# Optimization experiments

Measured on AMD Instinct MI355X. Metric: run time of the kernel, lower is better.

## Reference

```python
import jax, jax.numpy as jnp
import numpy as np

THR = 0.5      # span-selection threshold
K_SUBJ = 16    # max subject/object spans kept per sentence (padded)
K_OBJ = 8      # max object spans kept per (subject, relation)

# Greedy threshold-based span pairing: for each start position i with
# start_prob>THR, take the first unused j>=i with end_prob>THR (NMS-like).
# Returns fixed-size padded spans [K,2] (int32) and a validity mask [K].
def greedy_spans(sp, ep, K):
    S = sp.shape[0]
    idxs = jnp.arange(S, dtype=jnp.int32)
    def step(carry, i):
        used, count, spans, valid = carry
        gate = sp[i] > THR
        cand = (ep > THR) & (~used) & (idxs >= i)
        has = jnp.any(cand)
        j = jnp.argmax(cand).astype(jnp.int32)  # first True
        found = gate & has
        slot = jnp.minimum(count, K - 1)
        write = found & (count < K)
        pair = jnp.where(write, jnp.stack([i, j]).astype(jnp.int32), spans[slot])
        spans = spans.at[slot].set(pair)
        valid = valid.at[slot].set(valid[slot] | write)
        used = used.at[j].set(used[j] | found)
        count = count + found.astype(jnp.int32)
        return (used, count, spans, valid), None
    init = (jnp.zeros(S, bool), jnp.int32(0),
            jnp.zeros((K, 2), jnp.int32), jnp.zeros(K, bool))
    (_, _, spans, valid), _ = jax.lax.scan(step, init, idxs)
    return spans, valid


def _model(token_embs, hg, rel_embs, b_rel_transe, head_w, head_b,
           Wmats, Wbias, rproj_w, rproj_b, V_w, V_b):
    # head_w/head_b order: 0 start_subj, 1 end_subj, 2 b_start_obj, 3 b_end_obj,
    #                      4 start_obj, 5 end_obj, 6 b_start_subj, 7 b_end_subj
    # Wmats/Wbias order:   0 W_s, 1 W_r, 2 W_g, 3 W_x, 4 W_r_b, 5 W_g_b, 6 W_x_b, 7 W_x2
    sig = jax.nn.sigmoid
    head = lambda x, i: sig(x @ head_w[i] + head_b[i])        # H->1 sigmoid head
    lin = lambda x, i: x @ Wmats[i].T + Wbias[i]              # H->H linear

    # ---- first-level span scores + greedy extraction (forward & backward) ----
    sub_sp, sub_ep = head(token_embs, 0), head(token_embs, 1)   # [B,S]
    bob_sp, bob_ep = head(token_embs, 2), head(token_embs, 3)
    g = jax.vmap(lambda a, b: greedy_spans(a, b, K_SUBJ))
    subj_spans, subj_valid = g(sub_sp, sub_ep)                  # [B,K,2],[B,K]
    b_subj_spans, b_subj_valid = g(bob_sp, bob_ep)

    def gather(tok_b, spans, valid):  # mean of start/end token embeddings
        e = (tok_b[spans[:, 0]] + tok_b[spans[:, 1]]) * 0.5
        return e * valid[:, None].astype(tok_b.dtype)
    s_k = jax.vmap(gather)(token_embs, subj_spans, subj_valid)      # [B,K,H]
    b_s_k = jax.vmap(gather)(token_embs, b_subj_spans, b_subj_valid)
    s_k_w = lin(s_k, 0) * subj_valid[..., None]                     # W_s + mask
    b_s_k_w = lin(b_s_k, 0) * b_subj_valid[..., None]

    # ---- relation-aware attention context C = sum_s A[b,s,r] * x[b,s] ----
    b_rel = b_rel_transe @ rproj_w.T + rproj_b                      # r_proj
    def attend(rels, ir, ig, ix):
        e = jnp.tanh(lin(token_embs, ix)[:, :, None, :]             # [B,S,1,H]
                     + lin(hg, ig)[:, None, None, :]                # [B,1,1,H]
                     + lin(rels, ir)[None, None, :, :])             # [1,1,R,H]
        v = e @ V_w + V_b[0]                                        # [B,S,R]
        A = jax.nn.softmax(v, axis=1)                               # over seq
        return jnp.einsum('bsr,bsh->brh', A, token_embs)            # [B,R,H]
    C = attend(rel_embs, 1, 2, 3)
    b_C = attend(b_rel, 4, 5, 6)

    # Heads are linear, so distribute w over the sum instead of
    # materializing the [B,S,K,R,H] tensor.
    tok_mix = token_embs + lin(token_embs, 7)
    def pair_probs(Cmat, skw, i):
        t_tok = tok_mix @ head_w[i]                                 # [B,S]
        t_sub = skw @ head_w[i]                                     # [B,K]
        t_rel = Cmat @ head_w[i]                                    # [B,R]
        return sig(t_tok[:, :, None, None] + t_sub[:, None, :, None]
                   + t_rel[:, None, None, :] + head_b[i])           # [B,S,K,R]
    obj_sp, obj_ep = pair_probs(C, s_k_w, 4), pair_probs(C, s_k_w, 5)
    bsub_sp, bsub_ep = pair_probs(b_C, b_s_k_w, 6), pair_probs(b_C, b_s_k_w, 7)

    # ---- greedy object-span extraction per (batch, subject, relation) ----
    def triples(sp4, ep4, subj_ok):
        B_, S_, K_, R_ = sp4.shape
        fsp = sp4.transpose(0, 2, 3, 1).reshape(-1, S_)
        fep = ep4.transpose(0, 2, 3, 1).reshape(-1, S_)
        spans, valid = jax.vmap(lambda a, b: greedy_spans(a, b, K_OBJ))(fsp, fep)
        spans = spans.reshape(B_, K_, R_, K_OBJ, 2)
        valid = valid.reshape(B_, K_, R_, K_OBJ) & subj_ok[:, :, None, None]
        return spans, valid
    f_spans, f_valid = triples(obj_sp, obj_ep, subj_valid)
    bw_spans, bw_valid = triples(bsub_sp, bsub_ep, b_subj_valid)

    probs = jnp.stack([obj_sp, obj_ep, bsub_sp, bsub_ep])           # [4,B,S,K,R]
    return (probs, subj_spans, subj_valid, b_subj_spans, b_subj_valid,
            f_spans, f_valid, bw_spans, bw_valid)


def setup_inputs() -> dict:
    key = jax.random.key(0)
    ks = jax.random.split(key, 12)
    B, S, H, R, T = 8, 256, 768, 40, 80
    sc = H ** -0.5
    return {
        'token_embs': jax.random.normal(ks[0], (B, S, H), jnp.float32),
        'hg': jax.random.normal(ks[1], (B, H), jnp.float32),
        'rel_embs': jax.random.normal(ks[2], (R, H), jnp.float32),
        'b_rel_transe': jax.random.normal(ks[3], (R, T), jnp.float32),
        'head_w': jax.random.normal(ks[4], (8, H), jnp.float32) * sc,
        'head_b': jax.random.normal(ks[5], (8,), jnp.float32) * 0.1,
        'Wmats': jax.random.normal(ks[6], (8, H, H), jnp.float32) * sc,
        'Wbias': jax.random.normal(ks[7], (8, H), jnp.float32) * 0.02,
        'rproj_w': jax.random.normal(ks[8], (H, T), jnp.float32) * (T ** -0.5),
        'rproj_b': jax.random.normal(ks[9], (H,), jnp.float32) * 0.02,
        'V_w': jax.random.normal(ks[10], (H,), jnp.float32) * sc,
        'V_b': jax.random.normal(ks[11], (1,), jnp.float32) * 0.1,
    }


def reference(token_embs, hg, rel_embs, b_rel_transe, head_w, head_b,
              Wmats, Wbias, rproj_w, rproj_b, V_w, V_b):
    return _model(token_embs, hg, rel_embs, b_rel_transe, head_w, head_b,
                  Wmats, Wbias, rproj_w, rproj_b, V_w, V_b)
```

## Files before the change

### kernel.cpp

```cpp
#include <hip/hip_runtime.h>
#include <hip/hip_bf16.h>
#include <stdint.h>

#define Bc 8
#define Sc 256
#define Hc 768
#define Rc 40
#define Tc 80
#define KSc 16
#define KOc 8

#define OUT_SSP 5242880
#define OUT_SVA 5243136
#define OUT_BSP 5243264
#define OUT_BVA 5243520
#define OUT_FSP 5243648
#define OUT_FVA 5325568
#define OUT_WSP 5366528
#define OUT_WVA 5448448

#define CM_PS (16 * Rc * Hc)
#define BSH (Bc * Sc * Hc)

__device__ inline double wave_reduce_d(double v) {
#pragma unroll
  for (int o = 32; o; o >>= 1) v += __shfl_down(v, o, 64);
  return v;
}
__device__ inline float wave_reduce_f(float v) {
#pragma unroll
  for (int o = 32; o; o >>= 1) v += __shfl_down(v, o, 64);
  return v;
}

__global__ __launch_bounds__(256) void k_l03(const float* __restrict__ x,
                                             const float* __restrict__ head_w,
                                             const float* __restrict__ head_b,
                                             float* __restrict__ l03) {
  int bs = blockIdx.x * 4 + (threadIdx.x >> 6);
  int lane = threadIdx.x & 63;
  if (bs >= Bc * Sc) return;
  const float* xr = x + (size_t)bs * Hc;
  double acc[4] = {0.0, 0.0, 0.0, 0.0};
  for (int h = lane; h < Hc; h += 64) {
    double xv = (double)xr[h];
    acc[0] += xv * (double)head_w[h];
    acc[1] += xv * (double)head_w[Hc + h];
    acc[2] += xv * (double)head_w[2 * Hc + h];
    acc[3] += xv * (double)head_w[3 * Hc + h];
  }
#pragma unroll
  for (int i = 0; i < 4; ++i) {
    double a = wave_reduce_d(acc[i]);
    if (lane == 0) l03[i * (Bc * Sc) + bs] = (float)(a + (double)head_b[i]);
  }
}

__device__ inline int find_first(const uint64_t* epm, const uint64_t* used, int i) {
  int wi = i >> 6;
  uint64_t m = epm[wi] & ~used[wi] & (~0ull << (i & 63));
  if (m) return (wi << 6) + (__ffsll((unsigned long long)m) - 1);
  for (int w = wi + 1; w < 4; ++w) {
    uint64_t mm = epm[w] & ~used[w];
    if (mm) return (w << 6) + (__ffsll((unsigned long long)mm) - 1);
  }
  return -1;
}

__global__ __launch_bounds__(64) void k_greedy1(const float* __restrict__ l03,
                                                int* __restrict__ spans1, int* __restrict__ valid1,
                                                float* __restrict__ out) {
  int t = blockIdx.x;
  int dir = t >> 3, b = t & 7;
  int lane = threadIdx.x;
  const float* sp = l03 + (dir * 2) * (Bc * Sc) + b * Sc;
  const float* ep = sp + Bc * Sc;
  uint64_t spm[4], epm[4];
#pragma unroll
  for (int w = 0; w < 4; ++w) {
    spm[w] = __ballot(sp[w * 64 + lane] > 0.f);
    epm[w] = __ballot(ep[w * 64 + lane] > 0.f);
  }
  __shared__ int ssp0[KSc], ssp1[KSc], sva[KSc];
  if (lane < KSc) { ssp0[lane] = 0; ssp1[lane] = 0; sva[lane] = 0; }
  __syncthreads();
  if (lane == 0) {
    uint64_t used[4] = {0, 0, 0, 0};
    int cnt = 0;
#pragma unroll
    for (int w = 0; w < 4; ++w) {
      uint64_t g = spm[w];
      while (g) {
        int bit = __ffsll((unsigned long long)g) - 1;
        g &= g - 1;
        int i = w * 64 + bit;
        int j = find_first(epm, used, i);
        if (j < 0) continue;
        used[j >> 6] |= (1ull << (j & 63));
        if (cnt < KSc) { ssp0[cnt] = i; ssp1[cnt] = j; sva[cnt] = 1; }
        cnt++;
      }
    }
  }
  __syncthreads();
  int base = (dir * Bc + b) * KSc;
  float* osp = out + (dir ? OUT_BSP : OUT_SSP) + b * KSc * 2;
  float* ova = out + (dir ? OUT_BVA : OUT_SVA) + b * KSc;
  if (lane < KSc) {
    spans1[(base + lane) * 2] = ssp0[lane];
    spans1[(base + lane) * 2 + 1] = ssp1[lane];
    valid1[base + lane] = sva[lane];
    osp[lane * 2] = (float)ssp0[lane];
    osp[lane * 2 + 1] = (float)ssp1[lane];
    ova[lane] = (float)sva[lane];
  }
}

__global__ __launch_bounds__(256) void k_prep(const float* __restrict__ brt,
                                              const float* __restrict__ rw,
                                              const float* __restrict__ rb,
                                              const float* __restrict__ Wmats,
                                              const float* __restrict__ head_w,
                                              const float* __restrict__ x,
                                              const int* __restrict__ spans1,
                                              float* __restrict__ brel,
                                              double* __restrict__ hv,
                                              float* __restrict__ eb) {
  int bb = blockIdx.x;
  int tid = threadIdx.x;
  if (bb < 12) {
    int idx = bb * 256 + tid;
    int i = idx / Hc, j = idx % Hc;
    const float* h4 = head_w + (4 + i) * Hc;
    const float* W7 = Wmats + (size_t)7 * Hc * Hc;
    double acc = (double)h4[j];
    for (int hh = 0; hh < Hc; ++hh)
      acc += (double)W7[(size_t)hh * Hc + j] * (double)h4[hh];
    hv[idx] = acc;
  } else if (bb < 132) {
    int idx = (bb - 12) * 256 + tid;
    int r = idx / Hc, h = idx % Hc;
    float acc = rb[h];
    const float* a = brt + r * Tc;
    const float* w = rw + (size_t)h * Tc;
    for (int t = 0; t < Tc; ++t) acc = fmaf(a[t], w[t], acc);
    brel[idx] = acc;
  } else {
    int row = bb - 132;
    int b = (row / KSc) % Bc;
    int s0 = spans1[row * 2], s1 = spans1[row * 2 + 1];
    const float* x0 = x + ((size_t)b * Sc + s0) * Hc;
    const float* x1 = x + ((size_t)b * Sc + s1) * Hc;
    float* er = eb + (size_t)row * Hc;
    for (int h = tid; h < Hc; h += 256) er[h] = 0.5f * (x0[h] + x1[h]);
  }
}

__global__ __launch_bounds__(256) void k_skw(const float* __restrict__ eb,
                                             const float* __restrict__ Wmats,
                                             const float* __restrict__ Wbias,
                                             const int* __restrict__ valid1,
                                             float* __restrict__ skw) {
  int m0 = blockIdx.y * 32;
  int n0 = blockIdx.x * 64;
  __shared__ float Asl[32][36];
  __shared__ float Bsl[32][68];
  int tid = threadIdx.x;
  int arow = tid >> 3, acol = (tid & 7) << 2;
  int brow = tid >> 2, bcol = (tid & 3) << 2;
  int txi = tid & 15, tyi = tid >> 4;
  const float* ap = eb + (size_t)(m0 + arow) * Hc + acol;
  const float* bp = Wmats + (size_t)(n0 + brow) * Hc + bcol;
  int nb = n0 + txi * 4;
  float4 bias = *(const float4*)&Wbias[nb];
  float acc[2][4];
#pragma unroll
  for (int i = 0; i < 2; ++i) { acc[i][0] = bias.x; acc[i][1] = bias.y; acc[i][2] = bias.z; acc[i][3] = bias.w; }
  for (int k0 = 0; k0 < Hc; k0 += 32) {
    float4 av = *(const float4*)(ap + k0);
    float4 b0 = *(const float4*)(bp + k0);
    float4 b1 = *(const float4*)(bp + k0 + 16);
    __syncthreads();
    Asl[acol + 0][arow] = av.x; Asl[acol + 1][arow] = av.y; Asl[acol + 2][arow] = av.z; Asl[acol + 3][arow] = av.w;
    Bsl[bcol + 0][brow] = b0.x; Bsl[bcol + 1][brow] = b0.y; Bsl[bcol + 2][brow] = b0.z; Bsl[bcol + 3][brow] = b0.w;
    Bsl[bcol + 16][brow] = b1.x; Bsl[bcol + 17][brow] = b1.y; Bsl[bcol + 18][brow] = b1.z; Bsl[bcol + 19][brow] = b1.w;
    __syncthreads();
#pragma unroll
    for (int kk = 0; kk < 32; ++kk) {
      float a0 = Asl[kk][tyi * 2], a1 = Asl[kk][tyi * 2 + 1];
      float4 b = *(const float4*)&Bsl[kk][txi * 4];
      acc[0][0] = fmaf(a0, b.x, acc[0][0]); acc[0][1] = fmaf(a0, b.y, acc[0][1]);
      acc[0][2] = fmaf(a0, b.z, acc[0][2]); acc[0][3] = fmaf(a0, b.w, acc[0][3]);
      acc[1][0] = fmaf(a1, b.x, acc[1][0]); acc[1][1] = fmaf(a1, b.y, acc[1][1]);
      acc[1][2] = fmaf(a1, b.z, acc[1][2]); acc[1][3] = fmaf(a1, b.w, acc[1][3]);
    }
  }
  int m_ = m0 + tyi * 2;
#pragma unroll
  for (int i = 0; i < 2; ++i) {
    int v = valid1[m_ + i];
    float4 o;
    o.x = v ? acc[i][0] : 0.f; o.y = v ? acc[i][1] : 0.f;
    o.z = v ? acc[i][2] : 0.f; o.w = v ? acc[i][3] : 0.f;
    *(float4*)&skw[(size_t)(m_ + i) * Hc + nb] = o;
  }
}

__global__ __launch_bounds__(256) void k_tgtr(const float* __restrict__ hg,
                                              const float* __restrict__ rel,
                                              const float* __restrict__ brel,
                                              const float* __restrict__ Wmats,
                                              const float* __restrict__ Wbias,
                                              float* __restrict__ tg,
                                              float* __restrict__ tr) {
  int grp = blockIdx.z;
  const float* Asrc; int M; int wsel; float* dst;
  if (grp == 0)      { Asrc = hg;   M = 8;  wsel = 2; dst = tg; }
  else if (grp == 1) { Asrc = hg;   M = 8;  wsel = 5; dst = tg + 8 * Hc; }
  else if (grp == 2) { Asrc = rel;  M = 40; wsel = 1; dst = tr; }
  else               { Asrc = brel; M = 40; wsel = 4; dst = tr + 40 * Hc; }
  int m0 = blockIdx.y * 32;
  if (m0 >= M) return;
  int n0 = blockIdx.x * 64;
  const float* W = Wmats + (size_t)wsel * Hc * Hc;
  const float* bias = Wbias + wsel * Hc;
  __shared__ float Asl[32][36];
  __shared__ float Bsl[32][68];
  int tid = threadIdx.x;
  int arow = tid >> 3, acol = (tid & 7) << 2;
  int brow = tid >> 2, bcol = (tid & 3) << 2;
  int txi = tid & 15, tyi = tid >> 4;
  int ar = m0 + arow;
  const float* ap = Asrc + (size_t)(ar < M ? ar : 0) * Hc + acol;
  const float* bp = W + (size_t)(n0 + brow) * Hc + bcol;
  int nb = n0 + txi * 4;
  float4 bv = *(const float4*)&bias[nb];
  float acc[2][4];
#pragma unroll
  for (int i = 0; i < 2; ++i) { acc[i][0] = bv.x; acc[i][1] = bv.y; acc[i][2] = bv.z; acc[i][3] = bv.w; }
  for (int k0 = 0; k0 < Hc; k0 += 32) {
    float4 av = *(const float4*)(ap + k0);
    float4 b0 = *(const float4*)(bp + k0);
    float4 b1 = *(const float4*)(bp + k0 + 16);
    __syncthreads();
    Asl[acol + 0][arow] = av.x; Asl[acol + 1][arow] = av.y; Asl[acol + 2][arow] = av.z; Asl[acol + 3][arow] = av.w;
    Bsl[bcol + 0][brow] = b0.x; Bsl[bcol + 1][brow] = b0.y; Bsl[bcol + 2][brow] = b0.z; Bsl[bcol + 3][brow] = b0.w;
    Bsl[bcol + 16][brow] = b1.x; Bsl[bcol + 17][brow] = b1.y; Bsl[bcol + 18][brow] = b1.z; Bsl[bcol + 19][brow] = b1.w;
    __syncthreads();
#pragma unroll
    for (int kk = 0; kk < 32; ++kk) {
      float a0 = Asl[kk][tyi * 2], a1 = Asl[kk][tyi * 2 + 1];
      float4 b = *(const float4*)&Bsl[kk][txi * 4];
      acc[0][0] = fmaf(a0, b.x, acc[0][0]); acc[0][1] = fmaf(a0, b.y, acc[0][1]);
      acc[0][2] = fmaf(a0, b.z, acc[0][2]); acc[0][3] = fmaf(a0, b.w, acc[0][3]);
      acc[1][0] = fmaf(a1, b.x, acc[1][0]); acc[1][1] = fmaf(a1, b.y, acc[1][1]);
      acc[1][2] = fmaf(a1, b.z, acc[1][2]); acc[1][3] = fmaf(a1, b.w, acc[1][3]);
    }
  }
  int m_ = m0 + tyi * 2;
#pragma unroll
  for (int i = 0; i < 2; ++i) {
    if (m_ + i < M) {
      float4 o; o.x = acc[i][0]; o.y = acc[i][1]; o.z = acc[i][2]; o.w = acc[i][3];
      *(float4*)&dst[(size_t)(m_ + i) * Hc + nb] = o;
    }
  }
}

#define BM 64
#define BN 64
#define BKK 32
#define LDP 68
__global__ __launch_bounds__(256) void k_tx(const float* __restrict__ x,
                                            const float* __restrict__ Wmats,
                                            const float* __restrict__ Wbias,
                                            float* __restrict__ txo) {
  int dir = blockIdx.z;
  const float* W = Wmats + (size_t)(dir ? 6 : 3) * Hc * Hc;
  const float* bias = Wbias + (dir ? 6 : 3) * Hc;
  float* outp = txo + (size_t)dir * BSH;
  int m0 = blockIdx.y * BM;
  int n0 = blockIdx.x * BN;
  __shared__ float Asl[BKK][LDP];
  __shared__ float Bsl[BKK][LDP];
  int tid = threadIdx.x;
  int lr = tid >> 2;
  int lc = (tid & 3) << 2;
  int txi = tid & 15, tyi = tid >> 4;
  const float* xp = x + (size_t)(m0 + lr) * Hc + lc;
  const float* wp = W + (size_t)(n0 + lr) * Hc + lc;
  float4 a0 = *(const float4*)(xp);
  float4 a1 = *(const float4*)(xp + 16);
  float4 b0 = *(const float4*)(wp);
  float4 b1 = *(const float4*)(wp + 16);
  float acc[4][4] = {};
  for (int k0 = 0; k0 < Hc; k0 += BKK) {
    __syncthreads();
    Asl[lc + 0][lr] = a0.x; Asl[lc + 1][lr] = a0.y; Asl[lc + 2][lr] = a0.z; Asl[lc + 3][lr] = a0.w;
    Asl[lc + 16][lr] = a1.x; Asl[lc + 17][lr] = a1.y; Asl[lc + 18][lr] = a1.z; Asl[lc + 19][lr] = a1.w;
    Bsl[lc + 0][lr] = b0.x; Bsl[lc + 1][lr] = b0.y; Bsl[lc + 2][lr] = b0.z; Bsl[lc + 3][lr] = b0.w;
    Bsl[lc + 16][lr] = b1.x; Bsl[lc + 17][lr] = b1.y; Bsl[lc + 18][lr] = b1.z; Bsl[lc + 19][lr] = b1.w;
    __syncthreads();
    if (k0 + BKK < Hc) {
      a0 = *(const float4*)(xp + k0 + BKK);
      a1 = *(const float4*)(xp + k0 + BKK + 16);
      b0 = *(const float4*)(wp + k0 + BKK);
      b1 = *(const float4*)(wp + k0 + BKK + 16);
    }
#pragma unroll
    for (int kk = 0; kk < BKK; ++kk) {
      float4 a = *(const float4*)&Asl[kk][tyi * 4];
      float4 b = *(const float4*)&Bsl[kk][txi * 4];
      acc[0][0] = fmaf(a.x, b.x, acc[0][0]); acc[0][1] = fmaf(a.x, b.y, acc[0][1]);
      acc[0][2] = fmaf(a.x, b.z, acc[0][2]); acc[0][3] = fmaf(a.x, b.w, acc[0][3]);
      acc[1][0] = fmaf(a.y, b.x, acc[1][0]); acc[1][1] = fmaf(a.y, b.y, acc[1][1]);
      acc[1][2] = fmaf(a.y, b.z, acc[1][2]); acc[1][3] = fmaf(a.y, b.w, acc[1][3]);
      acc[2][0] = fmaf(a.z, b.x, acc[2][0]); acc[2][1] = fmaf(a.z, b.y, acc[2][1]);
      acc[2][2] = fmaf(a.z, b.z, acc[2][2]); acc[2][3] = fmaf(a.z, b.w, acc[2][3]);
      acc[3][0] = fmaf(a.w, b.x, acc[3][0]); acc[3][1] = fmaf(a.w, b.y, acc[3][1]);
      acc[3][2] = fmaf(a.w, b.z, acc[3][2]); acc[3][3] = fmaf(a.w, b.w, acc[3][3]);
    }
  }
  int nb = n0 + txi * 4;
  float4 bb = *(const float4*)&bias[nb];
#pragma unroll
  for (int i2 = 0; i2 < 4; ++i2) {
    float4 o;
    o.x = acc[i2][0] + bb.x; o.y = acc[i2][1] + bb.y;
    o.z = acc[i2][2] + bb.z; o.w = acc[i2][3] + bb.w;
    *(float4*)&outp[(size_t)(m0 + tyi * 4 + i2) * Hc + nb] = o;
  }
}

__global__ __launch_bounds__(256) void k_v(const float* __restrict__ txo,
                                           const float* __restrict__ tg,
                                           const float* __restrict__ tr,
                                           const float* __restrict__ Vw,
                                           const float* __restrict__ Vb,
                                           float* __restrict__ va) {
  const float Cl = 2.8853900817779268f;
  int id = blockIdx.x;
  int dir = id >> 10;
  int rem = id & 1023;
  int rhalf = rem & 1;
  int bs0 = (rem >> 1) * 4;
  int b = bs0 >> 8;
  int tid = threadIdx.x;
  int wv = tid >> 6, lane = tid & 63;
  const float* tgr = tg + (dir * Bc + b) * Hc;
  float xt[4][12], vw[12];
#pragma unroll
  for (int u = 0; u < 12; ++u) {
    int h = lane + 64 * u;
    vw[u] = Vw[h];
    float tgv = tgr[h];
#pragma unroll
    for (int si = 0; si < 4; ++si)
      xt[si][u] = (txo[((size_t)dir * (Bc * Sc) + bs0 + si) * Hc + h] + tgv) * Cl;
  }
  float vb0 = Vb[0];
  for (int q = 0; q < 5; ++q) {
    int r = rhalf * 20 + wv * 5 + q;
    const float* trr = tr + ((size_t)dir * Rc + r) * Hc + lane;
    float p0 = 0.f, p1 = 0.f, p2 = 0.f, p3 = 0.f;
#pragma unroll
    for (int u = 0; u < 12; ++u) {
      float t = trr[64 * u] * Cl;
      float e0 = __builtin_amdgcn_exp2f(xt[0][u] + t);
      float e1 = __builtin_amdgcn_exp2f(xt[1][u] + t);
      float e2 = __builtin_amdgcn_exp2f(xt[2][u] + t);
      float e3 = __builtin_amdgcn_exp2f(xt[3][u] + t);
      p0 = fmaf(fmaf(-2.f, __builtin_amdgcn_rcpf(e0 + 1.f), 1.f), vw[u], p0);
      p1 = fmaf(fmaf(-2.f, __builtin_amdgcn_rcpf(e1 + 1.f), 1.f), vw[u], p1);
      p2 = fmaf(fmaf(-2.f, __builtin_amdgcn_rcpf(e2 + 1.f), 1.f), vw[u], p2);
      p3 = fmaf(fmaf(-2.f, __builtin_amdgcn_rcpf(e3 + 1.f), 1.f), vw[u], p3);
    }
    p0 = wave_reduce_f(p0); p1 = wave_reduce_f(p1);
    p2 = wave_reduce_f(p2); p3 = wave_reduce_f(p3);
    if (lane == 0) {
      size_t base = ((size_t)dir * (Bc * Sc) + bs0) * Rc + r;
      va[base] = p0 + vb0;
      va[base + Rc] = p1 + vb0;
      va[base + 2 * Rc] = p2 + vb0;
      va[base + 3 * Rc] = p3 + vb0;
    }
  }
}

__global__ __launch_bounds__(256) void k_softmax(float* __restrict__ va) {
  int id = blockIdx.x;
  int dir = id / (Bc * Rc); int rem = id % (Bc * Rc);
  int b = rem / Rc; int r = rem % Rc;
  int s = threadIdx.x;
  float* base = va + (((size_t)dir * Bc + b) * Sc) * Rc + r;
  float v = base[(size_t)s * Rc];
  __shared__ float red[8];
  float m = v;
#pragma unroll
  for (int o = 32; o; o >>= 1) m = fmaxf(m, __shfl_xor(m, o, 64));
  if ((s & 63) == 0) red[s >> 6] = m;
  __syncthreads();
  if (s == 0) red[4] = fmaxf(fmaxf(red[0], red[1]), fmaxf(red[2], red[3]));
  __syncthreads();
  m = red[4];
  float e = expf(v - m);
  float t = e;
#pragma unroll
  for (int o = 32; o; o >>= 1) t += __shfl_xor(t, o, 64);
  __syncthreads();
  if ((s & 63) == 0) red[s >> 6] = t;
  __syncthreads();
  if (s == 0) red[4] = red[0] + red[1] + red[2] + red[3];
  __syncthreads();
  base[(size_t)s * Rc] = e / red[4];
}

__global__ __launch_bounds__(256, 1) void k_C(const float* __restrict__ va,
                                              const float* __restrict__ x,
                                              float* __restrict__ Cm4) {
  int id = blockIdx.x;
  int p = id & 3;
  int g = id >> 2;
  int b = g & 7;
  __shared__ float As_[64 * Rc];
  int tid = threadIdx.x;
  const float* vab = va + ((size_t)g * Sc + p * 64) * Rc;
  for (int idx = tid; idx < 64 * Rc; idx += 256) As_[idx] = vab[idx];
  __syncthreads();
  const float* xb = x + ((size_t)b * Sc + p * 64) * Hc;
  float acc[3][Rc];
#pragma unroll
  for (int j = 0; j < 3; ++j)
#pragma unroll
    for (int r = 0; r < Rc; ++r) acc[j][r] = 0.f;
  for (int s = 0; s < 64; ++s) {
    float xv0 = xb[(size_t)s * Hc + tid];
    float xv1 = xb[(size_t)s * Hc + 256 + tid];
    float xv2 = xb[(size_t)s * Hc + 512 + tid];
#pragma unroll
    for (int q = 0; q < 10; ++q) {
      float4 a4 = *(const float4*)&As_[s * Rc + q * 4];
      acc[0][q * 4 + 0] = fmaf(a4.x, xv0, acc[0][q * 4 + 0]);
      acc[0][q * 4 + 1] = fmaf(a4.y, xv0, acc[0][q * 4 + 1]);
      acc[0][q * 4 + 2] = fmaf(a4.z, xv0, acc[0][q * 4 + 2]);
      acc[0][q * 4 + 3] = fmaf(a4.w, xv0, acc[0][q * 4 + 3]);
      acc[1][q * 4 + 0] = fmaf(a4.x, xv1, acc[1][q * 4 + 0]);
      acc[1][q * 4 + 1] = fmaf(a4.y, xv1, acc[1][q * 4 + 1]);
      acc[1][q * 4 + 2] = fmaf(a4.z, xv1, acc[1][q * 4 + 2]);
      acc[1][q * 4 + 3] = fmaf(a4.w, xv1, acc[1][q * 4 + 3]);
      acc[2][q * 4 + 0] = fmaf(a4.x, xv2, acc[2][q * 4 + 0]);
      acc[2][q * 4 + 1] = fmaf(a4.y, xv2, acc[2][q * 4 + 1]);
      acc[2][q * 4 + 2] = fmaf(a4.z, xv2, acc[2][q * 4 + 2]);
      acc[2][q * 4 + 3] = fmaf(a4.w, xv2, acc[2][q * 4 + 3]);
    }
  }
#pragma unroll
  for (int r = 0; r < Rc; ++r) {
    size_t base = ((size_t)(p * 16 + g) * Rc + r) * Hc + tid;
    Cm4[base] = acc[0][r];
    Cm4[base + 256] = acc[1][r];
    Cm4[base + 512] = acc[2][r];
  }
}

__global__ __launch_bounds__(256) void k_tt(const float* __restrict__ x,
                                            const double* __restrict__ hv,
                                            double* __restrict__ tt) {
  int bs = blockIdx.x * 4 + (threadIdx.x >> 6);
  int lane = threadIdx.x & 63;
  if (bs >= Bc * Sc) return;
  const float* xr = x + (size_t)bs * Hc;
  double acc[4] = {0.0, 0.0, 0.0, 0.0};
  for (int h = lane; h < Hc; h += 64) {
    double xv = (double)xr[h];
    acc[0] += xv * hv[h];
    acc[1] += xv * hv[Hc + h];
    acc[2] += xv * hv[2 * Hc + h];
    acc[3] += xv * hv[3 * Hc + h];
  }
#pragma unroll
  for (int i = 0; i < 4; ++i) {
    double a = wave_reduce_d(acc[i]);
    if (lane == 0) tt[i * (Bc * Sc) + bs] = a;
  }
}

__global__ __launch_bounds__(256) void k_tsc(const float* __restrict__ skw,
                                             const float* __restrict__ Cm4,
                                             const float* __restrict__ head_w,
                                             const float* __restrict__ Wbias,
                                             double* __restrict__ ts,
                                             double* __restrict__ trl,
                                             double* __restrict__ c4) {
  int wave = blockIdx.x * 4 + (threadIdx.x >> 6);
  int lane = threadIdx.x & 63;
  const float* src; const float* w; double* dst;
  bool partial4 = false;
  if (wave < 512) {
    int p = wave >> 7, rem = wave & 127;
    int b = rem >> 4, k = rem & 15, dir = p >> 1;
    src = skw + (((size_t)(dir * Bc + b)) * KSc + k) * Hc;
    w = head_w + (4 + p) * Hc;
    dst = ts + (p * Bc + b) * KSc + k;
  } else if (wave < 1792) {
    int q = wave - 512;
    int p = q / 320, rem = q % 320;
    int b = rem / Rc, r = rem % Rc, dir = p >> 1;
    src = Cm4 + ((size_t)(dir * Bc + b) * Rc + r) * Hc;
    w = head_w + (4 + p) * Hc;
    dst = trl + (p * Bc + b) * Rc + r;
    partial4 = true;
  } else if (wave < 1796) {
    int p = wave - 1792;
    src = Wbias + 7 * Hc;
    w = head_w + (4 + p) * Hc;
    dst = c4 + p;
  } else return;
  double acc = 0.0;
  if (partial4) {
    for (int h = lane; h < Hc; h += 64) {
      double cs = (double)src[h] + (double)src[h + CM_PS] +
                  (double)src[h + 2 * CM_PS] + (double)src[h + 3 * CM_PS];
      acc += cs * (double)w[h];
    }
  } else {
    for (int h = lane; h < Hc; h += 64) acc += (double)src[h] * (double)w[h];
  }
  acc = wave_reduce_d(acc);
  if (lane == 0) *dst = acc;
}

__global__ __launch_bounds__(256) void k_probs(const double* __restrict__ tt,
                                               const double* __restrict__ ts,
                                               const double* __restrict__ trl,
                                               const double* __restrict__ c4,
                                               const float* __restrict__ head_b,
                                               float* __restrict__ out) {
  int id = blockIdx.x;
  int b = id >> 8, s = id & 255;
  (void)s;
  __shared__ double tsb[4][KSc];
  __shared__ double trb[4][Rc];
  __shared__ double basep[4];
  int tid = threadIdx.x;
  if (tid < 64) { int p = tid >> 4, k = tid & 15; tsb[p][k] = ts[(p * Bc + b) * KSc + k]; }
  if (tid < 160) { int p = tid / Rc, r = tid % Rc; trb[p][r] = trl[(p * Bc + b) * Rc + r]; }
  if (tid < 4) basep[tid] = tt[tid * (Bc * Sc) + id] + c4[tid] + (double)head_b[4 + tid];
  __syncthreads();
#pragma unroll
  for (int p = 0; p < 4; ++p) {
    double base = basep[p];
    float* op = out + ((size_t)(p * Bc) * Sc + id) * (KSc * Rc);
    for (int kr = tid; kr < KSc * Rc; kr += 256) {
      int k = kr / Rc, r = kr - k * Rc;
      double l = base + tsb[p][k] + trb[p][r];
      op[kr] = 1.f / (1.f + expf(-(float)l));
    }
  }
}

__global__ __launch_bounds__(256) void k_greedy2(const double* __restrict__ tt,
                                                 const double* __restrict__ ts,
                                                 const double* __restrict__ trl,
                                                 const double* __restrict__ c4,
                                                 const float* __restrict__ head_b,
                                                 const int* __restrict__ valid1,
                                                 float* __restrict__ out) {
  int gid = blockIdx.x * blockDim.x + threadIdx.x;
  if (gid >= 2 * Bc * KSc * Rc) return;
  int dir = gid / (Bc * KSc * Rc);
  int rem = gid % (Bc * KSc * Rc);
  int b = rem / (KSc * Rc);
  int kr = rem % (KSc * Rc);
  int k = kr / Rc, r = kr % Rc;
  int p0 = dir * 2, p1 = p0 + 1;
  double off0 = ts[(p0 * Bc + b) * KSc + k] + trl[(p0 * Bc + b) * Rc + r] + c4[p0] + (double)head_b[4 + p0];
  double off1 = ts[(p1 * Bc + b) * KSc + k] + trl[(p1 * Bc + b) * Rc + r] + c4[p1] + (double)head_b[4 + p1];
  const double* t0 = tt + p0 * (Bc * Sc) + b * Sc;
  const double* t1 = tt + p1 * (Bc * Sc) + b * Sc;
  uint64_t spm[4], epm[4], used[4] = {0, 0, 0, 0};
#pragma unroll
  for (int w = 0; w < 4; ++w) {
    uint64_t ms = 0, me = 0;
    for (int bit = 0; bit < 64; ++bit) {
      int s = w * 64 + bit;
      if (t0[s] + off0 > 0.0) ms |= (1ull << bit);
      if (t1[s] + off1 > 0.0) me |= (1ull << bit);
    }
    spm[w] = ms; epm[w] = me;
  }
  float* osp = out + (dir ? OUT_WSP : OUT_FSP) + (size_t)rem * KOc * 2;
  float* ova = out + (dir ? OUT_WVA : OUT_FVA) + (size_t)rem * KOc;
  for (int o = 0; o < KOc; ++o) { osp[o * 2] = 0.f; osp[o * 2 + 1] = 0.f; ova[o] = 0.f; }
  float sval = valid1[(dir * Bc + b) * KSc + k] ? 1.f : 0.f;
  int cnt = 0;
  for (int w = 0; w < 4; ++w) {
    uint64_t g = spm[w];
    while (g) {
      int bit = __ffsll((unsigned long long)g) - 1;
      g &= g - 1;
      int i = w * 64 + bit;
      int j = find_first(epm, used, i);
      if (j < 0) continue;
      used[j >> 6] |= (1ull << (j & 63));
      if (cnt < KOc) { osp[cnt * 2] = (float)i; osp[cnt * 2 + 1] = (float)j; ova[cnt] = sval; }
      cnt++;
    }
  }
}

extern "C" void kernel_launch(void* const* d_in, const int* in_sizes, int n_in,
                              void* d_out, int out_size, void* d_ws, size_t ws_size,
                              hipStream_t stream) {
  (void)in_sizes; (void)n_in; (void)out_size; (void)ws_size;
  const float* x = (const float*)d_in[0];
  const float* hg = (const float*)d_in[1];
  const float* rel = (const float*)d_in[2];
  const float* brt = (const float*)d_in[3];
  const float* head_w = (const float*)d_in[4];
  const float* head_b = (const float*)d_in[5];
  const float* Wmats = (const float*)d_in[6];
  const float* Wbias = (const float*)d_in[7];
  const float* rproj_w = (const float*)d_in[8];
  const float* rproj_b = (const float*)d_in[9];
  const float* Vw = (const float*)d_in[10];
  const float* Vb = (const float*)d_in[11];
  float* out = (float*)d_out;
  char* ws = (char*)d_ws;

  double* hv  = (double*)(ws + 0);
  double* c4  = (double*)(ws + 24576);
  double* tt  = (double*)(ws + 24608);
  double* ts  = (double*)(ws + 90144);
  double* trl = (double*)(ws + 94240);
  float* l03  = (float*)(ws + 104480);
  float* brel = (float*)(ws + 137248);
  float* tg   = (float*)(ws + 260128);
  float* tr   = (float*)(ws + 309280);
  float* txb  = (float*)(ws + 555040);
  float* va   = (float*)(ws + 13137952);
  float* skw  = (float*)(ws + 15759392);
  int* spans1 = (int*)(ws + 16545824);
  int* valid1 = (int*)(ws + 16547872);
  float* eb   = txb;
  float* Cm4  = txb;

  k_l03<<<512, 256, 0, stream>>>(x, head_w, head_b, l03);
  k_greedy1<<<16, 64, 0, stream>>>(l03, spans1, valid1, out);
  k_prep<<<388, 256, 0, stream>>>(brt, rproj_w, rproj_b, Wmats, head_w, x, spans1, brel, hv, eb);
  k_skw<<<dim3(12, 8), 256, 0, stream>>>(eb, Wmats, Wbias, valid1, skw);
  k_tgtr<<<dim3(12, 2, 4), 256, 0, stream>>>(hg, rel, brel, Wmats, Wbias, tg, tr);
  k_tx<<<dim3(12, 32, 2), 256, 0, stream>>>(x, Wmats, Wbias, txb);
  k_v<<<2048, 256, 0, stream>>>(txb, tg, tr, Vw, Vb, va);
  k_softmax<<<640, 256, 0, stream>>>(va);
  k_C<<<64, 256, 0, stream>>>(va, x, Cm4);
  k_tt<<<512, 256, 0, stream>>>(x, hv, tt);
  k_tsc<<<449, 256, 0, stream>>>(skw, Cm4, head_w, Wbias, ts, trl, c4);
  k_probs<<<2048, 256, 0, stream>>>(tt, ts, trl, c4, head_b, out);
  k_greedy2<<<40, 256, 0, stream>>>(tt, ts, trl, c4, head_b, valid1, out);
}
```

Before: 353.2 us.

## Fuse head dot-products, merge small GEMMs, split k_C, use fast sigmoid

Moves the hv and brel precomputation ahead of the token pass so the four start/end head logits and the four tt projections come from a single read of x in one kernel. The subject-span GEMM and the tg/tr GEMMs are merged into one launch, and the span gather becomes its own small kernel. k_C is split across twice as many blocks with half the accumulators each, and k_greedy2 uses 64-thread blocks to spread over more CUs. k_probs switches to hardware exp2/rcp intrinsics, which may shift sigmoid outputs slightly.

```diff
diff --git a/kernel.cpp b/kernel.cpp
--- a/kernel.cpp
+++ b/kernel.cpp
@@ -33,26 +33,66 @@
   return v;
 }
 
-__global__ __launch_bounds__(256) void k_l03(const float* __restrict__ x,
-                                             const float* __restrict__ head_w,
-                                             const float* __restrict__ head_b,
-                                             float* __restrict__ l03) {
+__global__ __launch_bounds__(256) void k_prep0(const float* __restrict__ brt,
+                                               const float* __restrict__ rw,
+                                               const float* __restrict__ rb,
+                                               const float* __restrict__ Wmats,
+                                               const float* __restrict__ head_w,
+                                               float* __restrict__ brel,
+                                               double* __restrict__ hv) {
+  int bb = blockIdx.x;
+  int tid = threadIdx.x;
+  if (bb < 12) {
+    int idx = bb * 256 + tid;
+    int i = idx / Hc, j = idx % Hc;
+    const float* h4 = head_w + (4 + i) * Hc;
+    const float* W7 = Wmats + (size_t)7 * Hc * Hc;
+    double acc = (double)h4[j];
+    for (int hh = 0; hh < Hc; ++hh)
+      acc += (double)W7[(size_t)hh * Hc + j] * (double)h4[hh];
+    hv[idx] = acc;
+  } else {
+    int idx = (bb - 12) * 256 + tid;
+    int r = idx / Hc, h = idx % Hc;
+    float acc = rb[h];
+    const float* a = brt + r * Tc;
+    const float* w = rw + (size_t)h * Tc;
+    for (int t = 0; t < Tc; ++t) acc = fmaf(a[t], w[t], acc);
+    brel[idx] = acc;
+  }
+}
+
+__global__ __launch_bounds__(256) void k_l03tt(const float* __restrict__ x,
+                                               const float* __restrict__ head_w,
+                                               const float* __restrict__ head_b,
+                                               const double* __restrict__ hv,
+                                               float* __restrict__ l03,
+                                               double* __restrict__ tt) {
   int bs = blockIdx.x * 4 + (threadIdx.x >> 6);
   int lane = threadIdx.x & 63;
   if (bs >= Bc * Sc) return;
   const float* xr = x + (size_t)bs * Hc;
-  double acc[4] = {0.0, 0.0, 0.0, 0.0};
+  double acc[8] = {0, 0, 0, 0, 0, 0, 0, 0};
   for (int h = lane; h < Hc; h += 64) {
     double xv = (double)xr[h];
     acc[0] += xv * (double)head_w[h];
     acc[1] += xv * (double)head_w[Hc + h];
     acc[2] += xv * (double)head_w[2 * Hc + h];
     acc[3] += xv * (double)head_w[3 * Hc + h];
+    acc[4] += xv * hv[h];
+    acc[5] += xv * hv[Hc + h];
+    acc[6] += xv * hv[2 * Hc + h];
+    acc[7] += xv * hv[3 * Hc + h];
   }
 #pragma unroll
   for (int i = 0; i < 4; ++i) {
     double a = wave_reduce_d(acc[i]);
     if (lane == 0) l03[i * (Bc * Sc) + bs] = (float)(a + (double)head_b[i]);
+  }
+#pragma unroll
+  for (int i = 0; i < 4; ++i) {
+    double a = wave_reduce_d(acc[4 + i]);
+    if (lane == 0) tt[i * (Bc * Sc) + bs] = a;
   }
 }
 
@@ -116,112 +156,40 @@
   }
 }
 
-__global__ __launch_bounds__(256) void k_prep(const float* __restrict__ brt,
-                                              const float* __restrict__ rw,
-                                              const float* __restrict__ rb,
-                                              const float* __restrict__ Wmats,
-                                              const float* __restrict__ head_w,
-                                              const float* __restrict__ x,
-                                              const int* __restrict__ spans1,
-                                              float* __restrict__ brel,
-                                              double* __restrict__ hv,
-                                              float* __restrict__ eb) {
+__global__ __launch_bounds__(256) void k_egather(const float* __restrict__ x,
+                                                 const int* __restrict__ spans1,
+                                                 float* __restrict__ eb) {
+  int row = blockIdx.x;
+  int b = (row / KSc) % Bc;
+  int s0 = spans1[row * 2], s1 = spans1[row * 2 + 1];
+  const float* x0 = x + ((size_t)b * Sc + s0) * Hc;
+  const float* x1 = x + ((size_t)b * Sc + s1) * Hc;
+  float* er = eb + (size_t)row * Hc;
+  for (int h = threadIdx.x; h < Hc; h += 256) er[h] = 0.5f * (x0[h] + x1[h]);
+}
+
+__global__ __launch_bounds__(256) void k_small(const float* __restrict__ eb,
+                                               const float* __restrict__ hg,
+                                               const float* __restrict__ rel,
+                                               const float* __restrict__ brel,
+                                               const float* __restrict__ Wmats,
+                                               const float* __restrict__ Wbias,
+                                               const int* __restrict__ valid1,
+                                               float* __restrict__ skw,
+                                               float* __restrict__ tg,
+                                               float* __restrict__ tr) {
   int bb = blockIdx.x;
-  int tid = threadIdx.x;
-  if (bb < 12) {
-    int idx = bb * 256 + tid;
-    int i = idx / Hc, j = idx % Hc;
-    const float* h4 = head_w + (4 + i) * Hc;
-    const float* W7 = Wmats + (size_t)7 * Hc * Hc;
-    double acc = (double)h4[j];
-    for (int hh = 0; hh < Hc; ++hh)
-      acc += (double)W7[(size_t)hh * Hc + j] * (double)h4[hh];
-    hv[idx] = acc;
-  } else if (bb < 132) {
-    int idx = (bb - 12) * 256 + tid;
-    int r = idx / Hc, h = idx % Hc;
-    float acc = rb[h];
-    const float* a = brt + r * Tc;
-    const float* w = rw + (size_t)h * Tc;
-    for (int t = 0; t < Tc; ++t) acc = fmaf(a[t], w[t], acc);
-    brel[idx] = acc;
+  const float* Asrc; int M; int wsel; float* dst; int m0, n0; bool msk = false;
+  if (bb < 96) {
+    Asrc = eb; M = 256; wsel = 0; dst = skw; msk = true;
+    m0 = (bb / 12) * 32; n0 = (bb % 12) * 64;
   } else {
-    int row = bb - 132;
-    int b = (row / KSc) % Bc;
-    int s0 = spans1[row * 2], s1 = spans1[row * 2 + 1];
-    const float* x0 = x + ((size_t)b * Sc + s0) * Hc;
-    const float* x1 = x + ((size_t)b * Sc + s1) * Hc;
-    float* er = eb + (size_t)row * Hc;
-    for (int h = tid; h < Hc; h += 256) er[h] = 0.5f * (x0[h] + x1[h]);
-  }
-}
-
-__global__ __launch_bounds__(256) void k_skw(const float* __restrict__ eb,
-                                             const float* __restrict__ Wmats,
-                                             const float* __restrict__ Wbias,
-                                             const int* __restrict__ valid1,
-                                             float* __restrict__ skw) {
-  int m0 = blockIdx.y * 32;
-  int n0 = blockIdx.x * 64;
-  __shared__ float Asl[32][36];
-  __shared__ float Bsl[32][68];
-  int tid = threadIdx.x;
-  int arow = tid >> 3, acol = (tid & 7) << 2;
-  int brow = tid >> 2, bcol = (tid & 3) << 2;
-  int txi = tid & 15, tyi = tid >> 4;
-  const float* ap = eb + (size_t)(m0 + arow) * Hc + acol;
-  const float* bp = Wmats + (size_t)(n0 + brow) * Hc + bcol;
-  int nb = n0 + txi * 4;
-  float4 bias = *(const float4*)&Wbias[nb];
-  float acc[2][4];
-#pragma unroll
-  for (int i = 0; i < 2; ++i) { acc[i][0] = bias.x; acc[i][1] = bias.y; acc[i][2] = bias.z; acc[i][3] = bias.w; }
-  for (int k0 = 0; k0 < Hc; k0 += 32) {
-    float4 av = *(const float4*)(ap + k0);
-    float4 b0 = *(const float4*)(bp + k0);
-    float4 b1 = *(const float4*)(bp + k0 + 16);
-    __syncthreads();
-    Asl[acol + 0][arow] = av.x; Asl[acol + 1][arow] = av.y; Asl[acol + 2][arow] = av.z; Asl[acol + 3][arow] = av.w;
-    Bsl[bcol + 0][brow] = b0.x; Bsl[bcol + 1][brow] = b0.y; Bsl[bcol + 2][brow] = b0.z; Bsl[bcol + 3][brow] = b0.w;
-    Bsl[bcol + 16][brow] = b1.x; Bsl[bcol + 17][brow] = b1.y; Bsl[bcol + 18][brow] = b1.z; Bsl[bcol + 19][brow] = b1.w;
-    __syncthreads();
-#pragma unroll
-    for (int kk = 0; kk < 32; ++kk) {
-      float a0 = Asl[kk][tyi * 2], a1 = Asl[kk][tyi * 2 + 1];
-      float4 b = *(const float4*)&Bsl[kk][txi * 4];
-      acc[0][0] = fmaf(a0, b.x, acc[0][0]); acc[0][1] = fmaf(a0, b.y, acc[0][1]);
-      acc[0][2] = fmaf(a0, b.z, acc[0][2]); acc[0][3] = fmaf(a0, b.w, acc[0][3]);
-      acc[1][0] = fmaf(a1, b.x, acc[1][0]); acc[1][1] = fmaf(a1, b.y, acc[1][1]);
-      acc[1][2] = fmaf(a1, b.z, acc[1][2]); acc[1][3] = fmaf(a1, b.w, acc[1][3]);
-    }
-  }
-  int m_ = m0 + tyi * 2;
-#pragma unroll
-  for (int i = 0; i < 2; ++i) {
-    int v = valid1[m_ + i];
-    float4 o;
-    o.x = v ? acc[i][0] : 0.f; o.y = v ? acc[i][1] : 0.f;
-    o.z = v ? acc[i][2] : 0.f; o.w = v ? acc[i][3] : 0.f;
-    *(float4*)&skw[(size_t)(m_ + i) * Hc + nb] = o;
-  }
-}
-
-__global__ __launch_bounds__(256) void k_tgtr(const float* __restrict__ hg,
-                                              const float* __restrict__ rel,
-                                              const float* __restrict__ brel,
-                                              const float* __restrict__ Wmats,
-                                              const float* __restrict__ Wbias,
-                                              float* __restrict__ tg,
-                                              float* __restrict__ tr) {
-  int grp = blockIdx.z;
-  const float* Asrc; int M; int wsel; float* dst;
-  if (grp == 0)      { Asrc = hg;   M = 8;  wsel = 2; dst = tg; }
-  else if (grp == 1) { Asrc = hg;   M = 8;  wsel = 5; dst = tg + 8 * Hc; }
-  else if (grp == 2) { Asrc = rel;  M = 40; wsel = 1; dst = tr; }
-  else               { Asrc = brel; M = 40; wsel = 4; dst = tr + 40 * Hc; }
-  int m0 = blockIdx.y * 32;
-  if (m0 >= M) return;
-  int n0 = blockIdx.x * 64;
+    int q = bb - 96;
+    if (q < 12)      { Asrc = hg;   M = 8;  wsel = 2; dst = tg;           m0 = 0; n0 = q * 64; }
+    else if (q < 24) { Asrc = hg;   M = 8;  wsel = 5; dst = tg + 8 * Hc;  m0 = 0; n0 = (q - 12) * 64; }
+    else if (q < 48) { int qq = q - 24; Asrc = rel;  M = 40; wsel = 1; dst = tr;           m0 = (qq / 12) * 32; n0 = (qq % 12) * 64; }
+    else             { int qq = q - 48; Asrc = brel; M = 40; wsel = 4; dst = tr + 40 * Hc; m0 = (qq / 12) * 32; n0 = (qq % 12) * 64; }
+  }
   const float* W = Wmats + (size_t)wsel * Hc * Hc;
   const float* bias = Wbias + wsel * Hc;
   __shared__ float Asl[32][36];
@@ -260,9 +228,16 @@
   int m_ = m0 + tyi * 2;
 #pragma unroll
   for (int i = 0; i < 2; ++i) {
-    if (m_ + i < M) {
+    int mrow = m_ + i;
+    if (msk) {
+      int v = valid1[mrow];
+      float4 o;
+      o.x = v ? acc[i][0] : 0.f; o.y = v ? acc[i][1] : 0.f;
+      o.z = v ? acc[i][2] : 0.f; o.w = v ? acc[i][3] : 0.f;
+      *(float4*)&dst[(size_t)mrow * Hc + nb] = o;
+    } else if (mrow < M) {
       float4 o; o.x = acc[i][0]; o.y = acc[i][1]; o.z = acc[i][2]; o.w = acc[i][3];
-      *(float4*)&dst[(size_t)(m_ + i) * Hc + nb] = o;
+      *(float4*)&dst[(size_t)mrow * Hc + nb] = o;
     }
   }
 }
@@ -419,8 +394,9 @@
                                               const float* __restrict__ x,
                                               float* __restrict__ Cm4) {
   int id = blockIdx.x;
-  int p = id & 3;
-  int g = id >> 2;
+  int rr = id & 1;
+  int p = (id >> 1) & 3;
+  int g = id >> 3;
   int b = g & 7;
   __shared__ float As_[64 * Rc];
   int tid = threadIdx.x;
@@ -428,18 +404,19 @@
   for (int idx = tid; idx < 64 * Rc; idx += 256) As_[idx] = vab[idx];
   __syncthreads();
   const float* xb = x + ((size_t)b * Sc + p * 64) * Hc;
-  float acc[3][Rc];
+  float acc[3][20];
 #pragma unroll
   for (int j = 0; j < 3; ++j)
 #pragma unroll
-    for (int r = 0; r < Rc; ++r) acc[j][r] = 0.f;
+    for (int r = 0; r < 20; ++r) acc[j][r] = 0.f;
+  int rbase = rr * 20;
   for (int s = 0; s < 64; ++s) {
     float xv0 = xb[(size_t)s * Hc + tid];
     float xv1 = xb[(size_t)s * Hc + 256 + tid];
     float xv2 = xb[(size_t)s * Hc + 512 + tid];
 #pragma unroll
-    for (int q = 0; q < 10; ++q) {
-      float4 a4 = *(const float4*)&As_[s * Rc + q * 4];
+    for (int q = 0; q < 5; ++q) {
+      float4 a4 = *(const float4*)&As_[s * Rc + rbase + q * 4];
       acc[0][q * 4 + 0] = fmaf(a4.x, xv0, acc[0][q * 4 + 0]);
       acc[0][q * 4 + 1] = fmaf(a4.y, xv0, acc[0][q * 4 + 1]);
       acc[0][q * 4 + 2] = fmaf(a4.z, xv0, acc[0][q * 4 + 2]);
@@ -455,33 +432,11 @@
     }
   }
 #pragma unroll
-  for (int r = 0; r < Rc; ++r) {
-    size_t base = ((size_t)(p * 16 + g) * Rc + r) * Hc + tid;
+  for (int r = 0; r < 20; ++r) {
+    size_t base = ((size_t)(p * 16 + g) * Rc + rbase + r) * Hc + tid;
     Cm4[base] = acc[0][r];
     Cm4[base + 256] = acc[1][r];
     Cm4[base + 512] = acc[2][r];
-  }
-}
-
-__global__ __launch_bounds__(256) void k_tt(const float* __restrict__ x,
-                                            const double* __restrict__ hv,
-                                            double* __restrict__ tt) {
-  int bs = blockIdx.x * 4 + (threadIdx.x >> 6);
-  int lane = threadIdx.x & 63;
-  if (bs >= Bc * Sc) return;
-  const float* xr = x + (size_t)bs * Hc;
-  double acc[4] = {0.0, 0.0, 0.0, 0.0};
-  for (int h = lane; h < Hc; h += 64) {
-    double xv = (double)xr[h];
-    acc[0] += xv * hv[h];
-    acc[1] += xv * hv[Hc + h];
-    acc[2] += xv * hv[2 * Hc + h];
-    acc[3] += xv * hv[3 * Hc + h];
-  }
-#pragma unroll
-  for (int i = 0; i < 4; ++i) {
-    double a = wave_reduce_d(acc[i]);
-    if (lane == 0) tt[i * (Bc * Sc) + bs] = a;
   }
 }
 
@@ -536,6 +491,7 @@
                                                const double* __restrict__ c4,
                                                const float* __restrict__ head_b,
                                                float* __restrict__ out) {
+  const float L2E = 1.4426950408889634f;
   int id = blockIdx.x;
   int b = id >> 8, s = id & 255;
   (void)s;
@@ -553,20 +509,21 @@
     float* op = out + ((size_t)(p * Bc) * Sc + id) * (KSc * Rc);
     for (int kr = tid; kr < KSc * Rc; kr += 256) {
       int k = kr / Rc, r = kr - k * Rc;
-      double l = base + tsb[p][k] + trb[p][r];
-      op[kr] = 1.f / (1.f + expf(-(float)l));
-    }
-  }
-}
-
-__global__ __launch_bounds__(256) void k_greedy2(const double* __restrict__ tt,
-                                                 const double* __restrict__ ts,
-                                                 const double* __restrict__ trl,
-                                                 const double* __restrict__ c4,
-                                                 const float* __restrict__ head_b,
-                                                 const int* __restrict__ valid1,
-                                                 float* __restrict__ out) {
-  int gid = blockIdx.x * blockDim.x + threadIdx.x;
+      float l = (float)(base + tsb[p][k] + trb[p][r]);
+      float e = __builtin_amdgcn_exp2f(-L2E * l);
+      op[kr] = __builtin_amdgcn_rcpf(1.f + e);
+    }
+  }
+}
+
+__global__ __launch_bounds__(64) void k_greedy2(const double* __restrict__ tt,
+                                                const double* __restrict__ ts,
+                                                const double* __restrict__ trl,
+                                                const double* __restrict__ c4,
+                                                const float* __restrict__ head_b,
+                                                const int* __restrict__ valid1,
+                                                float* __restrict__ out) {
+  int gid = blockIdx.x * 64 + threadIdx.x;
   if (gid >= 2 * Bc * KSc * Rc) return;
   int dir = gid / (Bc * KSc * Rc);
   int rem = gid % (Bc * KSc * Rc);
@@ -645,17 +602,16 @@
   float* eb   = txb;
   float* Cm4  = txb;
 
-  k_l03<<<512, 256, 0, stream>>>(x, head_w, head_b, l03);
+  k_prep0<<<132, 256, 0, stream>>>(brt, rproj_w, rproj_b, Wmats, head_w, brel, hv);
+  k_l03tt<<<512, 256, 0, stream>>>(x, head_w, head_b, hv, l03, tt);
   k_greedy1<<<16, 64, 0, stream>>>(l03, spans1, valid1, out);
-  k_prep<<<388, 256, 0, stream>>>(brt, rproj_w, rproj_b, Wmats, head_w, x, spans1, brel, hv, eb);
-  k_skw<<<dim3(12, 8), 256, 0, stream>>>(eb, Wmats, Wbias, valid1, skw);
-  k_tgtr<<<dim3(12, 2, 4), 256, 0, stream>>>(hg, rel, brel, Wmats, Wbias, tg, tr);
+  k_egather<<<256, 256, 0, stream>>>(x, spans1, eb);
+  k_small<<<168, 256, 0, stream>>>(eb, hg, rel, brel, Wmats, Wbias, valid1, skw, tg, tr);
   k_tx<<<dim3(12, 32, 2), 256, 0, stream>>>(x, Wmats, Wbias, txb);
   k_v<<<2048, 256, 0, stream>>>(txb, tg, tr, Vw, Vb, va);
   k_softmax<<<640, 256, 0, stream>>>(va);
-  k_C<<<64, 256, 0, stream>>>(va, x, Cm4);
-  k_tt<<<512, 256, 0, stream>>>(x, hv, tt);
+  k_C<<<128, 256, 0, stream>>>(va, x, Cm4);
   k_tsc<<<449, 256, 0, stream>>>(skw, Cm4, head_w, Wbias, ts, trl, c4);
   k_probs<<<2048, 256, 0, stream>>>(tt, ts, trl, c4, head_b, out);
-  k_greedy2<<<40, 256, 0, stream>>>(tt, ts, trl, c4, head_b, valid1, out);
-}
+  k_greedy2<<<160, 64, 0, stream>>>(tt, ts, trl, c4, head_b, valid1, out);
+}
```

Result: faster. 310.3 us, median of 2 (-12.2%).
